# Optimization experiments

Hardware: AMD Instinct MI355X
Metric: run time of the kernel (lower is better)

Reference implementation:

```python
import jax, jax.numpy as jnp
import numpy as np

NF, NH, NC, B = 8, 200, 8, 131072  # nFeatures, nHidden, nCls, batch
NEQ = 2

def _lin_init(k, fan_in, fan_out):
    k1, k2 = jax.random.split(k)
    s = 1.0 / np.sqrt(fan_in)
    W = jax.random.uniform(k1, (fan_out, fan_in), minval=-s, maxval=s, dtype=jnp.float32)
    b = jax.random.uniform(k2, (fan_out,), minval=-s, maxval=s, dtype=jnp.float32)
    return W, b

def setup_inputs() -> dict:
    key = jax.random.key(0)
    ks = jax.random.split(key, 6)
    W0, b0 = _lin_init(ks[0], NF, NF)
    W1, b1 = _lin_init(ks[1], NF, NH)
    W2, b2 = _lin_init(ks[2], NH, NH)
    W3, b3 = _lin_init(ks[3], NH, NH)
    W4, b4 = _lin_init(ks[4], NH, NC)
    Q = jnp.eye(NF, dtype=jnp.float32)  # Parameter initialized to identity
    x = jax.random.normal(ks[5], (B, NF), dtype=jnp.float32)
    return dict(x=x, Q=Q, W0=W0, b0=b0, W1=W1, b1=b1, W2=W2, b2=b2, W3=W3, b3=b3, W4=W4, b4=b4)

def _qp_equality(Q, p, A, bvec):
    # min 1/2 z'Qz + p'z  s.t.  A z = b.  (G=0, h=0 => inequality constraints vacuous.)
    # KKT: [Q A'; A 0] [z; nu] = [-p; b], solved batched (tiny 10x10 systems).
    Bn, m, n = A.shape
    Qb = jnp.broadcast_to(Q, (Bn, n, n))
    K = jnp.concatenate([
        jnp.concatenate([Qb, jnp.swapaxes(A, 1, 2)], axis=2),        # [B, n, n+m]
        jnp.concatenate([A, jnp.zeros((Bn, m, m), Q.dtype)], axis=2) # [B, m, n+m]
    ], axis=1)                                                        # [B, n+m, n+m]
    rhs = jnp.concatenate([-p, bvec], axis=1)                         # [B, n+m]
    sol = jnp.linalg.solve(K, rhs[..., None])[..., 0]
    return sol[:, :n]

def reference(x, Q, W0, b0, W1, b1, W2, b2, W3, b3, W4, b4):
    h = x @ W0.T + b0                      # fc0, [B, 8]
    p = -h
    z_ = jnp.zeros_like(h[:, 3])
    o_ = jnp.ones_like(h[:, 3])
    # A[i] = [[0,0,0,0,h[i,3],1,0,0], [0,0,0,0,0,0,h[i,3],1]]  (detached in original)
    A = jnp.stack([
        jnp.stack([z_, z_, z_, z_, h[:, 3], o_, z_, z_], axis=1),
        jnp.stack([z_, z_, z_, z_, z_, z_, h[:, 3], o_], axis=1)], axis=1)  # [B, 2, 8]
    A = jax.lax.stop_gradient(A)  # torch.tensor(...) breaks the graph for A
    bvec = jnp.stack([h[:, 3] * h[:, 4] + h[:, 5],
                      h[:, 3] * h[:, 6] + h[:, 7]], axis=1)  # [B, 2]
    z = _qp_equality(Q, p, A, bvec)        # QPFunction solution, [B, 8]
    y = jax.nn.relu(z @ W1.T + b1)
    y = jax.nn.relu(y @ W2.T + b2)
    y = jax.nn.relu(y @ W3.T + b3)
    return y @ W4.T + b4                   # [B, 8]
```

## Files before the change

kernel.cpp:

```cpp
#include <hip/hip_runtime.h>
#include <math.h>

typedef _Float16 f16;
typedef f16 half8 __attribute__((ext_vector_type(8)));
typedef float floatx4 __attribute__((ext_vector_type(4)));

#define NF 8
#define NH 200
#define NC 8
#define ACT_W 232
#define ROWS 64
#define CHUNK 4
#define OUTP_W 9
#define FRAG 512

#define WS_QI   0
#define WS_B1P  256
#define WS_B2P  1152
#define WS_B3P  2048
#define WS_WP1  3008
#define WS_WP2  16320
#define WS_WP3  109504
#define WS_WP4  202688
#define WS_NEED 212000

__device__ __forceinline__ void pack_frag(const float* __restrict__ W, int Nv, int Kv,
                                          int nkt, int nks, f16* __restrict__ dst, int gid)
{
    if (gid < nks * nkt * 64) {
        const int ks    = gid / (nkt * 64);
        const int rem   = gid - ks * nkt * 64;
        const int nt    = rem >> 6;
        const int lane  = rem & 63;
        const int n     = nt * 16 + (lane & 15);
        const int kbase = ks * 32 + ((lane >> 4) * 8);
        f16 tmp[8];
#pragma unroll
        for (int j = 0; j < 8; ++j) {
            const int k = kbase + j;
            tmp[j] = (n < Nv && k < Kv) ? (f16)W[n * Kv + k] : (f16)0.0f;
        }
        *(half8*)&dst[(size_t)gid * 8] = *(const half8*)tmp;
    }
}

__global__ void prep_kernel(const float* __restrict__ Q,
                            const float* __restrict__ W1, const float* __restrict__ b1,
                            const float* __restrict__ W2, const float* __restrict__ b2,
                            const float* __restrict__ W3, const float* __restrict__ b3,
                            const float* __restrict__ W4,
                            char* __restrict__ ws)
{
    const int gid = blockIdx.x * 256 + threadIdx.x;
    pack_frag(W1, NH, NF, 13, 1, (f16*)(ws + WS_WP1), gid);
    pack_frag(W2, NH, NH, 13, 7, (f16*)(ws + WS_WP2), gid);
    pack_frag(W3, NH, NH, 13, 7, (f16*)(ws + WS_WP3), gid);
    pack_frag(W4, NC, NH, 1,  7, (f16*)(ws + WS_WP4), gid);
    if (gid < 224) {
        ((float*)(ws + WS_B1P))[gid] = (gid < NH) ? b1[gid] : 0.0f;
        ((float*)(ws + WS_B2P))[gid] = (gid < NH) ? b2[gid] : 0.0f;
        ((float*)(ws + WS_B3P))[gid] = (gid < NH) ? b3[gid] : 0.0f;
    }

    if (blockIdx.x == 0) {
        __shared__ float aug[8][16];
        __shared__ int piv;
        float* Qi = (float*)(ws + WS_QI);
        const int t  = threadIdx.x;
        const bool a = t < 128;
        const int r  = (t >> 4) & 7;
        const int c2 = t & 15;
        if (a) aug[r][c2] = (c2 < 8) ? Q[r * 8 + c2] : ((c2 - 8 == r) ? 1.0f : 0.0f);
        __syncthreads();
        for (int c = 0; c < 8; ++c) {
            if (t == 0) {
                int p = c; float best = fabsf(aug[c][c]);
                for (int rr = c + 1; rr < 8; ++rr) {
                    float v = fabsf(aug[rr][c]);
                    if (v > best) { best = v; p = rr; }
                }
                piv = p;
            }
            __syncthreads();
            const int p = piv;
            float myv = a ? aug[r][c2] : 0.0f;
            __syncthreads();
            if (a) {
                if (r == c)      aug[p][c2] = myv;
                else if (r == p) aug[c][c2] = myv;
            }
            __syncthreads();
            const float pv = aug[c][c];
            __syncthreads();
            if (a && r == c) aug[r][c2] = aug[r][c2] / pv;
            __syncthreads();
            const float fac  = (a && r != c) ? aug[r][c] : 0.0f;
            const float prow = aug[c][c2];
            __syncthreads();
            if (a) aug[r][c2] -= fac * prow;
            __syncthreads();
        }
        if (a && c2 >= 8) Qi[r * 8 + (c2 - 8)] = aug[r][c2];
    }
}

__device__ __forceinline__ half8 ldf(const f16* __restrict__ p, int lane)
{
    return *(const half8*)&p[lane * 8];
}

template<int TC>
__device__ __forceinline__ void run_path(
    const float* __restrict__ x,
    const float* __restrict__ W0, const float* __restrict__ b0,
    const float* __restrict__ b4,
    const char* __restrict__ ws,
    float* __restrict__ out, int B,
    f16* __restrict__ actA, f16* __restrict__ actB,
    f16* __restrict__ zbuf, float* __restrict__ outP,
    const int wid, const int lane, const int c, const int g, const int t0)
{
    const float* Qi  = (const float*)(ws + WS_QI);
    const float* b1p = (const float*)(ws + WS_B1P);
    const float* b2p = (const float*)(ws + WS_B2P);
    const float* b3p = (const float*)(ws + WS_B3P);
    const f16*  Wp1  = (const f16*)(ws + WS_WP1);
    const f16*  Wp2  = (const f16*)(ws + WS_WP2);
    const f16*  Wp3  = (const f16*)(ws + WS_WP3);
    const f16*  Wp4  = (const f16*)(ws + WS_WP4);

    half8 wf1[TC], wf2[TC][7], wf3[TC][7];
    float bv1[TC], bv2[TC], bv3[TC];
#pragma unroll
    for (int t = 0; t < TC; ++t) {
        wf1[t] = ldf(Wp1 + (size_t)(t0 + t) * FRAG, lane);
#pragma unroll
        for (int ks = 0; ks < 7; ++ks) {
            wf2[t][ks] = ldf(Wp2 + (size_t)(ks * 13 + t0 + t) * FRAG, lane);
            wf3[t][ks] = ldf(Wp3 + (size_t)(ks * 13 + t0 + t) * FRAG, lane);
        }
        bv1[t] = b1p[(t0 + t) * 16 + c];
        bv2[t] = b2p[(t0 + t) * 16 + c];
        bv3[t] = b3p[(t0 + t) * 16 + c];
    }
    const bool doL4 = (wid < 7);
    half8 w4f = {};
    if (doL4) w4f = ldf(Wp4 + (size_t)wid * FRAG, lane);

    const long blockbase = (long)blockIdx.x * (ROWS * CHUNK);
    const int  tid = wid * 64 + lane;

    if (tid < 256) {
        f16* buf = (tid & 128) ? actB : actA;
        const int row  = (tid >> 1) & 63;
        const int part = tid & 1;
        half8 zz = {};
        *(half8*)&buf[row * ACT_W + 208 + part * 8] = zz;
    }

    float xr[NF];
#pragma unroll
    for (int i = 0; i < NF; ++i) xr[i] = 0.0f;
    if (wid == 0) {
        const long gr = blockbase + lane;
        if (gr < B) {
            const float4* xp = (const float4*)(x + gr * NF);
            const float4 A = xp[0], Bv = xp[1];
            xr[0] = A.x; xr[1] = A.y; xr[2] = A.z; xr[3] = A.w;
            xr[4] = Bv.x; xr[5] = Bv.y; xr[6] = Bv.z; xr[7] = Bv.w;
        }
    }

#pragma unroll 1
    for (int ck = 0; ck < CHUNK; ++ck) {
        const long base = blockbase + (long)ck * ROWS;

        if (wid == 0) {
            float xn[NF];
#pragma unroll
            for (int i = 0; i < NF; ++i) xn[i] = 0.0f;
            if (ck + 1 < CHUNK) {
                const long gn = base + ROWS + lane;
                if (gn < B) {
                    const float4* xp = (const float4*)(x + gn * NF);
                    const float4 A = xp[0], Bv = xp[1];
                    xn[0] = A.x; xn[1] = A.y; xn[2] = A.z; xn[3] = A.w;
                    xn[4] = Bv.x; xn[5] = Bv.y; xn[6] = Bv.z; xn[7] = Bv.w;
                }
            }
            float h[NF];
#pragma unroll
            for (int j = 0; j < NF; ++j) {
                float acc = b0[j];
#pragma unroll
                for (int k = 0; k < NF; ++k) acc = fmaf(W0[j * NF + k], xr[k], acc);
                h[j] = acc;
            }
            float tq[NF], u0[NF], u1[NF];
            const float h3 = h[3];
#pragma unroll
            for (int i = 0; i < NF; ++i) {
                float s = 0.0f;
#pragma unroll
                for (int k = 0; k < NF; ++k) s = fmaf(Qi[i * NF + k], h[k], s);
                tq[i] = s;
                u0[i] = fmaf(Qi[i * NF + 4], h3, Qi[i * NF + 5]);
                u1[i] = fmaf(Qi[i * NF + 6], h3, Qi[i * NF + 7]);
            }
            const float m00 = fmaf(h3, u0[4], u0[5]);
            const float m01 = fmaf(h3, u1[4], u1[5]);
            const float m10 = fmaf(h3, u0[6], u0[7]);
            const float m11 = fmaf(h3, u1[6], u1[7]);
            const float r0  = fmaf(h3, tq[4], tq[5]) - fmaf(h3, h[4], h[5]);
            const float r1  = fmaf(h3, tq[6], tq[7]) - fmaf(h3, h[6], h[7]);
            const float idet = 1.0f / (m00 * m11 - m01 * m10);
            const float nu0 = (m11 * r0 - m01 * r1) * idet;
            const float nu1 = (m00 * r1 - m10 * r0) * idet;
            half8 zh, zz = {};
#pragma unroll
            for (int k = 0; k < 8; ++k) zh[k] = (f16)(tq[k] - u0[k] * nu0 - u1[k] * nu1);
            *(half8*)&zbuf[lane * 32 + 0]  = zh;
            *(half8*)&zbuf[lane * 32 + 8]  = zz;
            *(half8*)&zbuf[lane * 32 + 16] = zz;
            *(half8*)&zbuf[lane * 32 + 24] = zz;
#pragma unroll
            for (int i = 0; i < NF; ++i) xr[i] = xn[i];
        }
        __syncthreads();

#pragma unroll
        for (int m = 0; m < 4; ++m) {
            const half8 az = *(const half8*)&zbuf[(m * 16 + c) * 32 + g * 8];
#pragma unroll
            for (int t = 0; t < TC; ++t) {
                floatx4 acc;
                acc[0] = bv1[t]; acc[1] = bv1[t]; acc[2] = bv1[t]; acc[3] = bv1[t];
                acc = __builtin_amdgcn_mfma_f32_16x16x32_f16(az, wf1[t], acc, 0, 0, 0);
#pragma unroll
                for (int r = 0; r < 4; ++r)
                    actA[(m * 16 + g * 4 + r) * ACT_W + (t0 + t) * 16 + c] =
                        (f16)fmaxf(acc[r], 0.0f);
            }
        }
        __syncthreads();

#pragma unroll
        for (int m = 0; m < 4; ++m) {
            half8 af[7];
#pragma unroll
            for (int ks = 0; ks < 7; ++ks)
                af[ks] = *(const half8*)&actA[(m * 16 + c) * ACT_W + ks * 32 + g * 8];
#pragma unroll
            for (int t = 0; t < TC; ++t) {
                floatx4 acc;
                acc[0] = bv2[t]; acc[1] = bv2[t]; acc[2] = bv2[t]; acc[3] = bv2[t];
#pragma unroll
                for (int ks = 0; ks < 7; ++ks)
                    acc = __builtin_amdgcn_mfma_f32_16x16x32_f16(af[ks], wf2[t][ks], acc, 0, 0, 0);
#pragma unroll
                for (int r = 0; r < 4; ++r)
                    actB[(m * 16 + g * 4 + r) * ACT_W + (t0 + t) * 16 + c] =
                        (f16)fmaxf(acc[r], 0.0f);
            }
        }
        __syncthreads();

#pragma unroll
        for (int m = 0; m < 4; ++m) {
            half8 af[7];
#pragma unroll
            for (int ks = 0; ks < 7; ++ks)
                af[ks] = *(const half8*)&actB[(m * 16 + c) * ACT_W + ks * 32 + g * 8];
#pragma unroll
            for (int t = 0; t < TC; ++t) {
                floatx4 acc;
                acc[0] = bv3[t]; acc[1] = bv3[t]; acc[2] = bv3[t]; acc[3] = bv3[t];
#pragma unroll
                for (int ks = 0; ks < 7; ++ks)
                    acc = __builtin_amdgcn_mfma_f32_16x16x32_f16(af[ks], wf3[t][ks], acc, 0, 0, 0);
#pragma unroll
                for (int r = 0; r < 4; ++r)
                    actA[(m * 16 + g * 4 + r) * ACT_W + (t0 + t) * 16 + c] =
                        (f16)fmaxf(acc[r], 0.0f);
            }
        }
        __syncthreads();

        if (doL4) {
#pragma unroll
            for (int m = 0; m < 4; ++m) {
                const half8 af = *(const half8*)&actA[(m * 16 + c) * ACT_W + wid * 32 + g * 8];
                floatx4 a4 = {};
                a4 = __builtin_amdgcn_mfma_f32_16x16x32_f16(af, w4f, a4, 0, 0, 0);
                if (c < NC) {
#pragma unroll
                    for (int r = 0; r < 4; ++r)
                        outP[(wid * ROWS + m * 16 + g * 4 + r) * OUTP_W + c] = a4[r];
                }
            }
        }
        __syncthreads();

        if (tid < 256) {
            const int e   = tid * 2;
            const int row = e >> 3;
            const int col = e & 7;
            float s0 = b4[col], s1 = b4[col + 1];
#pragma unroll
            for (int w = 0; w < 7; ++w) {
                s0 += outP[(w * ROWS + row) * OUTP_W + col];
                s1 += outP[(w * ROWS + row) * OUTP_W + col + 1];
            }
            const long gr = base + row;
            if (gr < B) {
                float2 v; v.x = s0; v.y = s1;
                *(float2*)&out[gr * NC + col] = v;
            }
        }
    }
}

__global__ __launch_bounds__(512, 2)
void mlp_pers(const float* __restrict__ x,
              const float* __restrict__ W0, const float* __restrict__ b0,
              const float* __restrict__ b4,
              const char* __restrict__ ws,
              float* __restrict__ out, int B)
{
    __shared__ f16   actA[ROWS * ACT_W];
    __shared__ f16   actB[ROWS * ACT_W];
    __shared__ f16   zbuf[ROWS * 32];
    __shared__ float outP[7 * ROWS * OUTP_W];

    const int tid  = threadIdx.x;
    const int lane = tid & 63;
    const int wid  = __builtin_amdgcn_readfirstlane(tid >> 6);
    const int c    = lane & 15;
    const int g    = lane >> 4;

    if (wid < 5)
        run_path<2>(x, W0, b0, b4, ws, out, B, actA, actB, zbuf, outP,
                    wid, lane, c, g, 2 * wid);
    else
        run_path<1>(x, W0, b0, b4, ws, out, B, actA, actB, zbuf, outP,
                    wid, lane, c, g, wid + 5);
}

#define BT 64
#define NWAVE 8
#define JB 25
#define CH 8

__device__ __forceinline__ void layer200(const float* __restrict__ in_,
                                         float* __restrict__ out_,
                                         const float* __restrict__ W,
                                         const float* __restrict__ bias,
                                         int j0, int lane)
{
    float acc[JB];
#pragma unroll
    for (int jj = 0; jj < JB; ++jj) acc[jj] = bias[j0 + jj];
#pragma unroll 1
    for (int k0 = 0; k0 < NH; k0 += CH) {
        float a[CH];
#pragma unroll
        for (int u = 0; u < CH; ++u) a[u] = in_[(k0 + u) * BT + lane];
#pragma unroll
        for (int jj = 0; jj < JB; ++jj) {
            const float* wr = W + (j0 + jj) * NH + k0;
#pragma unroll
            for (int u = 0; u < CH; ++u) acc[jj] = fmaf(wr[u], a[u], acc[jj]);
        }
    }
#pragma unroll
    for (int jj = 0; jj < JB; ++jj)
        out_[(j0 + jj) * BT + lane] = fmaxf(acc[jj], 0.0f);
}

__global__ void qinv_kernel(const float* __restrict__ Q, float* __restrict__ Qi)
{
    __shared__ float aug[8][16];
    __shared__ int piv;
    const int t  = threadIdx.x;
    const int r  = t >> 4;
    const int c2 = t & 15;
    aug[r][c2] = (c2 < 8) ? Q[r * 8 + c2] : ((c2 - 8 == r) ? 1.0f : 0.0f);
    __syncthreads();
    for (int c = 0; c < 8; ++c) {
        if (t == 0) {
            int p = c; float best = fabsf(aug[c][c]);
            for (int rr = c + 1; rr < 8; ++rr) {
                float v = fabsf(aug[rr][c]);
                if (v > best) { best = v; p = rr; }
            }
            piv = p;
        }
        __syncthreads();
        const int p = piv;
        float myv = aug[r][c2];
        __syncthreads();
        if (r == c)      aug[p][c2] = myv;
        else if (r == p) aug[c][c2] = myv;
        __syncthreads();
        const float pv = aug[c][c];
        __syncthreads();
        if (r == c) aug[r][c2] = aug[r][c2] / pv;
        __syncthreads();
        const float fac  = (r == c) ? 0.0f : aug[r][c];
        const float prow = aug[c][c2];
        __syncthreads();
        aug[r][c2] -= fac * prow;
        __syncthreads();
    }
    if (c2 >= 8) Qi[r * 8 + (c2 - 8)] = aug[r][c2];
}

__global__ __launch_bounds__(BT * NWAVE, 2)
void mlp_fused(const float* __restrict__ x, const float* __restrict__ Qi,
               const float* __restrict__ W0, const float* __restrict__ b0,
               const float* __restrict__ W1, const float* __restrict__ b1,
               const float* __restrict__ W2, const float* __restrict__ b2,
               const float* __restrict__ W3, const float* __restrict__ b3,
               const float* __restrict__ W4, const float* __restrict__ b4,
               float* __restrict__ out, int B)
{
    __shared__ float actA[NH * BT];
    __shared__ float actB[NH * BT];
    __shared__ float outP[NWAVE * NC * BT];

    const int lane = threadIdx.x & 63;
    const int wid  = __builtin_amdgcn_readfirstlane((int)(threadIdx.x >> 6));
    const int g    = blockIdx.x * BT + lane;
    const int j0   = wid * JB;

    float xr[NF];
    if (g < B) {
        const float4* xp = reinterpret_cast<const float4*>(x + (size_t)g * NF);
        float4 x0 = xp[0], x1 = xp[1];
        xr[0] = x0.x; xr[1] = x0.y; xr[2] = x0.z; xr[3] = x0.w;
        xr[4] = x1.x; xr[5] = x1.y; xr[6] = x1.z; xr[7] = x1.w;
    } else {
#pragma unroll
        for (int i = 0; i < NF; ++i) xr[i] = 0.0f;
    }
    float h[NF];
#pragma unroll
    for (int j = 0; j < NF; ++j) {
        float acc = b0[j];
#pragma unroll
        for (int k = 0; k < NF; ++k) acc = fmaf(W0[j * NF + k], xr[k], acc);
        h[j] = acc;
    }
    float tq[NF], u0[NF], u1[NF];
    const float h3 = h[3];
#pragma unroll
    for (int i = 0; i < NF; ++i) {
        float s = 0.0f;
#pragma unroll
        for (int k = 0; k < NF; ++k) s = fmaf(Qi[i * NF + k], h[k], s);
        tq[i] = s;
        u0[i] = fmaf(Qi[i * NF + 4], h3, Qi[i * NF + 5]);
        u1[i] = fmaf(Qi[i * NF + 6], h3, Qi[i * NF + 7]);
    }
    const float m00 = fmaf(h3, u0[4], u0[5]);
    const float m01 = fmaf(h3, u1[4], u1[5]);
    const float m10 = fmaf(h3, u0[6], u0[7]);
    const float m11 = fmaf(h3, u1[6], u1[7]);
    const float r0  = fmaf(h3, tq[4], tq[5]) - fmaf(h3, h[4], h[5]);
    const float r1  = fmaf(h3, tq[6], tq[7]) - fmaf(h3, h[6], h[7]);
    const float idet = 1.0f / (m00 * m11 - m01 * m10);
    const float nu0 = (m11 * r0 - m01 * r1) * idet;
    const float nu1 = (m00 * r1 - m10 * r0) * idet;
    float z[NF];
#pragma unroll
    for (int i = 0; i < NF; ++i) z[i] = tq[i] - u0[i] * nu0 - u1[i] * nu1;

#pragma unroll
    for (int jj = 0; jj < JB; ++jj) {
        const int j = j0 + jj;
        float acc = b1[j];
#pragma unroll
        for (int k = 0; k < NF; ++k) acc = fmaf(W1[j * NF + k], z[k], acc);
        actA[j * BT + lane] = fmaxf(acc, 0.0f);
    }
    __syncthreads();
    layer200(actA, actB, W2, b2, j0, lane);
    __syncthreads();
    layer200(actB, actA, W3, b3, j0, lane);
    __syncthreads();
    {
        float a[JB];
#pragma unroll
        for (int kk = 0; kk < JB; ++kk) a[kk] = actA[(j0 + kk) * BT + lane];
        float acc[NC];
#pragma unroll
        for (int o = 0; o < NC; ++o) acc[o] = 0.0f;
#pragma unroll
        for (int o = 0; o < NC; ++o) {
            const float* wr = W4 + o * NH + j0;
#pragma unroll
            for (int kk = 0; kk < JB; ++kk) acc[o] = fmaf(wr[kk], a[kk], acc[o]);
        }
#pragma unroll
        for (int o = 0; o < NC; ++o) outP[(wid * NC + o) * BT + lane] = acc[o];
    }
    __syncthreads();
    {
        float s = b4[wid];
#pragma unroll
        for (int w = 0; w < NWAVE; ++w) s += outP[(w * NC + wid) * BT + lane];
        if (g < B) out[(size_t)g * NC + wid] = s;
    }
}

extern "C" void kernel_launch(void* const* d_in, const int* in_sizes, int n_in,
                              void* d_out, int out_size, void* d_ws, size_t ws_size,
                              hipStream_t stream)
{
    const float* x  = (const float*)d_in[0];
    const float* Q  = (const float*)d_in[1];
    const float* W0 = (const float*)d_in[2];
    const float* b0 = (const float*)d_in[3];
    const float* W1 = (const float*)d_in[4];
    const float* b1 = (const float*)d_in[5];
    const float* W2 = (const float*)d_in[6];
    const float* b2 = (const float*)d_in[7];
    const float* W3 = (const float*)d_in[8];
    const float* b3 = (const float*)d_in[9];
    const float* W4 = (const float*)d_in[10];
    const float* b4 = (const float*)d_in[11];
    float* out = (float*)d_out;

    const int B = in_sizes[0] / NF;

    if (ws_size >= WS_NEED) {
        hipLaunchKernelGGL(prep_kernel, dim3(23), dim3(256), 0, stream,
                           Q, W1, b1, W2, b2, W3, b3, W4, (char*)d_ws);
        const int nblk = (B + ROWS * CHUNK - 1) / (ROWS * CHUNK);
        hipLaunchKernelGGL(mlp_pers, dim3(nblk), dim3(512), 0, stream,
                           x, W0, b0, b4, (const char*)d_ws, out, B);
    } else {
        float* Qi = (float*)d_ws;
        hipLaunchKernelGGL(qinv_kernel, dim3(1), dim3(128), 0, stream, Q, Qi);
        hipLaunchKernelGGL(mlp_fused, dim3((B + BT - 1) / BT), dim3(BT * NWAVE), 0, stream,
                           x, Qi, W0, b0, W1, b1, W2, b2, W3, b3, W4, b4, out, B);
    }
}
```

Baseline: 57.71 us.

## Switch MLP layers to 32x32x16 MFMA with 128-row tiles and swizzled LDS

Replaces the 16x16x32 MFMA path with 32x32x16 MFMA tiles, where each of 7 waves owns a 32-column slice of the hidden layer. Weights are repacked in the prep kernel to match. Rows per chunk double to 128, and activation stores and loads use an XOR swizzle to avoid LDS bank conflicts. The goal is better MFMA efficiency, with register-resident weights reused over more rows and two accumulators interleaved to hide MFMA latency. The cost is higher register and LDS pressure: LDS nearly doubles, which may cap occupancy at 2 blocks per CU.

```diff
diff --git a/kernel.cpp b/kernel.cpp
--- a/kernel.cpp
+++ b/kernel.cpp
@@ -4,12 +4,14 @@
 typedef _Float16 f16;
 typedef f16 half8 __attribute__((ext_vector_type(8)));
 typedef float floatx4 __attribute__((ext_vector_type(4)));
+typedef float floatx16 __attribute__((ext_vector_type(16)));
 
 #define NF 8
 #define NH 200
 #define NC 8
 #define ACT_W 232
-#define ROWS 64
+#define ZB_W 40
+#define ROWS 128
 #define CHUNK 4
 #define OUTP_W 9
 #define FRAG 512
@@ -18,11 +20,11 @@
 #define WS_B1P  256
 #define WS_B2P  1152
 #define WS_B3P  2048
-#define WS_WP1  3008
-#define WS_WP2  16320
-#define WS_WP3  109504
-#define WS_WP4  202688
-#define WS_NEED 212000
+#define WS_W1P  2944
+#define WS_W2P  10112
+#define WS_W3P  110464
+#define WS_W4P  210816
+#define WS_NEED 217984
 
 __device__ __forceinline__ void pack_frag(const float* __restrict__ W, int Nv, int Kv,
                                           int nkt, int nks, f16* __restrict__ dst, int gid)
@@ -44,6 +46,26 @@
     }
 }
 
+__device__ __forceinline__ void pack32(const float* __restrict__ W, int Nv, int Kv,
+                                       int nks, f16* __restrict__ dst, int gid)
+{
+    if (gid < nks * 7 * 64) {
+        const int ks    = gid / 448;
+        const int rem   = gid - ks * 448;
+        const int nt    = rem >> 6;
+        const int lane  = rem & 63;
+        const int n     = nt * 32 + (lane & 31);
+        const int kbase = ks * 16 + ((lane >> 5) * 8);
+        f16 tmp[8];
+#pragma unroll
+        for (int j = 0; j < 8; ++j) {
+            const int k = kbase + j;
+            tmp[j] = (n < Nv && k < Kv) ? (f16)W[n * Kv + k] : (f16)0.0f;
+        }
+        *(half8*)&dst[(size_t)gid * 8] = *(const half8*)tmp;
+    }
+}
+
 __global__ void prep_kernel(const float* __restrict__ Q,
                             const float* __restrict__ W1, const float* __restrict__ b1,
                             const float* __restrict__ W2, const float* __restrict__ b2,
@@ -52,10 +74,10 @@
                             char* __restrict__ ws)
 {
     const int gid = blockIdx.x * 256 + threadIdx.x;
-    pack_frag(W1, NH, NF, 13, 1, (f16*)(ws + WS_WP1), gid);
-    pack_frag(W2, NH, NH, 13, 7, (f16*)(ws + WS_WP2), gid);
-    pack_frag(W3, NH, NH, 13, 7, (f16*)(ws + WS_WP3), gid);
-    pack_frag(W4, NC, NH, 1,  7, (f16*)(ws + WS_WP4), gid);
+    pack32(W1, NH, NF, 1,  (f16*)(ws + WS_W1P), gid);
+    pack32(W2, NH, NH, 14, (f16*)(ws + WS_W2P), gid);
+    pack32(W3, NH, NH, 14, (f16*)(ws + WS_W3P), gid);
+    pack_frag(W4, NC, NH, 1, 7, (f16*)(ws + WS_W4P), gid);
     if (gid < 224) {
         ((float*)(ws + WS_B1P))[gid] = (gid < NH) ? b1[gid] : 0.0f;
         ((float*)(ws + WS_B2P))[gid] = (gid < NH) ? b2[gid] : 0.0f;
@@ -109,60 +131,65 @@
     return *(const half8*)&p[lane * 8];
 }
 
-template<int TC>
-__device__ __forceinline__ void run_path(
-    const float* __restrict__ x,
-    const float* __restrict__ W0, const float* __restrict__ b0,
-    const float* __restrict__ b4,
-    const char* __restrict__ ws,
-    float* __restrict__ out, int B,
-    f16* __restrict__ actA, f16* __restrict__ actB,
-    f16* __restrict__ zbuf, float* __restrict__ outP,
-    const int wid, const int lane, const int c, const int g, const int t0)
-{
+__global__ __launch_bounds__(448, 2)
+void mlp32(const float* __restrict__ x,
+           const float* __restrict__ W0, const float* __restrict__ b0,
+           const float* __restrict__ b4,
+           const char* __restrict__ ws,
+           float* __restrict__ out, int B)
+{
+    __shared__ f16   actA[ROWS * ACT_W];
+    __shared__ f16   actB[ROWS * ACT_W];
+    __shared__ f16   zbuf[ROWS * ZB_W];
+    __shared__ float outP[7 * ROWS * OUTP_W];
+
+    const int tid  = threadIdx.x;
+    const int lane = tid & 63;
+    const int wid  = __builtin_amdgcn_readfirstlane(tid >> 6);
+    const int l31  = lane & 31;
+    const int h    = lane >> 5;
+    const int c    = lane & 15;
+    const int g    = lane >> 4;
+    const int s    = (l31 >> 3) & 3;
+
     const float* Qi  = (const float*)(ws + WS_QI);
     const float* b1p = (const float*)(ws + WS_B1P);
     const float* b2p = (const float*)(ws + WS_B2P);
     const float* b3p = (const float*)(ws + WS_B3P);
-    const f16*  Wp1  = (const f16*)(ws + WS_WP1);
-    const f16*  Wp2  = (const f16*)(ws + WS_WP2);
-    const f16*  Wp3  = (const f16*)(ws + WS_WP3);
-    const f16*  Wp4  = (const f16*)(ws + WS_WP4);
-
-    half8 wf1[TC], wf2[TC][7], wf3[TC][7];
-    float bv1[TC], bv2[TC], bv3[TC];
-#pragma unroll
-    for (int t = 0; t < TC; ++t) {
-        wf1[t] = ldf(Wp1 + (size_t)(t0 + t) * FRAG, lane);
-#pragma unroll
-        for (int ks = 0; ks < 7; ++ks) {
-            wf2[t][ks] = ldf(Wp2 + (size_t)(ks * 13 + t0 + t) * FRAG, lane);
-            wf3[t][ks] = ldf(Wp3 + (size_t)(ks * 13 + t0 + t) * FRAG, lane);
-        }
-        bv1[t] = b1p[(t0 + t) * 16 + c];
-        bv2[t] = b2p[(t0 + t) * 16 + c];
-        bv3[t] = b3p[(t0 + t) * 16 + c];
-    }
-    const bool doL4 = (wid < 7);
-    half8 w4f = {};
-    if (doL4) w4f = ldf(Wp4 + (size_t)wid * FRAG, lane);
+    const f16*  W1p  = (const f16*)(ws + WS_W1P);
+    const f16*  W2p  = (const f16*)(ws + WS_W2P);
+    const f16*  W3p  = (const f16*)(ws + WS_W3P);
+    const f16*  W4p  = (const f16*)(ws + WS_W4P);
+
+    half8 wf2[14], wf3[14];
+#pragma unroll
+    for (int ks = 0; ks < 14; ++ks) {
+        wf2[ks] = ldf(W2p + (size_t)(ks * 7 + wid) * FRAG, lane);
+        wf3[ks] = ldf(W3p + (size_t)(ks * 7 + wid) * FRAG, lane);
+    }
+    const half8 wf1 = ldf(W1p + (size_t)wid * FRAG, lane);
+    const half8 w4f = ldf(W4p + (size_t)wid * FRAG, lane);
+    const float bv1 = b1p[wid * 32 + l31];
+    const float bv2 = b2p[wid * 32 + l31];
+    const float bv3 = b3p[wid * 32 + l31];
+
+    if (tid < 256) {
+        const int row = tid & 127;
+        f16* buf = (tid & 128) ? actB : actA;
+        const int sw = (row >> 3) & 3;
+        half8 zz = {};
+        *(half8*)&buf[row * ACT_W + ((26 ^ sw) << 3)] = zz;
+        *(half8*)&buf[row * ACT_W + ((27 ^ sw) << 3)] = zz;
+    }
 
     const long blockbase = (long)blockIdx.x * (ROWS * CHUNK);
-    const int  tid = wid * 64 + lane;
-
-    if (tid < 256) {
-        f16* buf = (tid & 128) ? actB : actA;
-        const int row  = (tid >> 1) & 63;
-        const int part = tid & 1;
-        half8 zz = {};
-        *(half8*)&buf[row * ACT_W + 208 + part * 8] = zz;
-    }
+    const int  hrow = wid * 64 + lane;
 
     float xr[NF];
 #pragma unroll
     for (int i = 0; i < NF; ++i) xr[i] = 0.0f;
-    if (wid == 0) {
-        const long gr = blockbase + lane;
+    if (wid < 2) {
+        const long gr = blockbase + hrow;
         if (gr < B) {
             const float4* xp = (const float4*)(x + gr * NF);
             const float4 A = xp[0], Bv = xp[1];
@@ -175,12 +202,12 @@
     for (int ck = 0; ck < CHUNK; ++ck) {
         const long base = blockbase + (long)ck * ROWS;
 
-        if (wid == 0) {
+        if (wid < 2) {
             float xn[NF];
 #pragma unroll
             for (int i = 0; i < NF; ++i) xn[i] = 0.0f;
             if (ck + 1 < CHUNK) {
-                const long gn = base + ROWS + lane;
+                const long gn = base + ROWS + hrow;
                 if (gn < B) {
                     const float4* xp = (const float4*)(x + gn * NF);
                     const float4 A = xp[0], Bv = xp[1];
@@ -188,22 +215,22 @@
                     xn[4] = Bv.x; xn[5] = Bv.y; xn[6] = Bv.z; xn[7] = Bv.w;
                 }
             }
-            float h[NF];
+            float hh[NF];
 #pragma unroll
             for (int j = 0; j < NF; ++j) {
                 float acc = b0[j];
 #pragma unroll
                 for (int k = 0; k < NF; ++k) acc = fmaf(W0[j * NF + k], xr[k], acc);
-                h[j] = acc;
+                hh[j] = acc;
             }
             float tq[NF], u0[NF], u1[NF];
-            const float h3 = h[3];
+            const float h3 = hh[3];
 #pragma unroll
             for (int i = 0; i < NF; ++i) {
-                float s = 0.0f;
-#pragma unroll
-                for (int k = 0; k < NF; ++k) s = fmaf(Qi[i * NF + k], h[k], s);
-                tq[i] = s;
+                float ss = 0.0f;
+#pragma unroll
+                for (int k = 0; k < NF; ++k) ss = fmaf(Qi[i * NF + k], hh[k], ss);
+                tq[i] = ss;
                 u0[i] = fmaf(Qi[i * NF + 4], h3, Qi[i * NF + 5]);
                 u1[i] = fmaf(Qi[i * NF + 6], h3, Qi[i * NF + 7]);
             }
@@ -211,18 +238,16 @@
             const float m01 = fmaf(h3, u1[4], u1[5]);
             const float m10 = fmaf(h3, u0[6], u0[7]);
             const float m11 = fmaf(h3, u1[6], u1[7]);
-            const float r0  = fmaf(h3, tq[4], tq[5]) - fmaf(h3, h[4], h[5]);
-            const float r1  = fmaf(h3, tq[6], tq[7]) - fmaf(h3, h[6], h[7]);
+            const float r0  = fmaf(h3, tq[4], tq[5]) - fmaf(h3, hh[4], hh[5]);
+            const float r1  = fmaf(h3, tq[6], tq[7]) - fmaf(h3, hh[6], hh[7]);
             const float idet = 1.0f / (m00 * m11 - m01 * m10);
             const float nu0 = (m11 * r0 - m01 * r1) * idet;
             const float nu1 = (m00 * r1 - m10 * r0) * idet;
             half8 zh, zz = {};
 #pragma unroll
             for (int k = 0; k < 8; ++k) zh[k] = (f16)(tq[k] - u0[k] * nu0 - u1[k] * nu1);
-            *(half8*)&zbuf[lane * 32 + 0]  = zh;
-            *(half8*)&zbuf[lane * 32 + 8]  = zz;
-            *(half8*)&zbuf[lane * 32 + 16] = zz;
-            *(half8*)&zbuf[lane * 32 + 24] = zz;
+            *(half8*)&zbuf[hrow * ZB_W + 0] = zh;
+            *(half8*)&zbuf[hrow * ZB_W + 8] = zz;
 #pragma unroll
             for (int i = 0; i < NF; ++i) xr[i] = xn[i];
         }
@@ -230,120 +255,109 @@
 
 #pragma unroll
         for (int m = 0; m < 4; ++m) {
-            const half8 az = *(const half8*)&zbuf[(m * 16 + c) * 32 + g * 8];
-#pragma unroll
-            for (int t = 0; t < TC; ++t) {
-                floatx4 acc;
-                acc[0] = bv1[t]; acc[1] = bv1[t]; acc[2] = bv1[t]; acc[3] = bv1[t];
-                acc = __builtin_amdgcn_mfma_f32_16x16x32_f16(az, wf1[t], acc, 0, 0, 0);
-#pragma unroll
-                for (int r = 0; r < 4; ++r)
-                    actA[(m * 16 + g * 4 + r) * ACT_W + (t0 + t) * 16 + c] =
-                        (f16)fmaxf(acc[r], 0.0f);
+            const half8 az = *(const half8*)&zbuf[(m * 32 + l31) * ZB_W + h * 8];
+            floatx16 a0;
+#pragma unroll
+            for (int i = 0; i < 16; ++i) a0[i] = bv1;
+            a0 = __builtin_amdgcn_mfma_f32_32x32x16_f16(az, wf1, a0, 0, 0, 0);
+            const int chunkw = wid * 4 + (l31 >> 3);
+#pragma unroll
+            for (int rr = 0; rr < 16; ++rr) {
+                const int row = m * 32 + (rr & 3) + 8 * (rr >> 2) + 4 * h;
+                actA[row * ACT_W + (((chunkw ^ (rr >> 2)) << 3) | (l31 & 7))] =
+                    (f16)fmaxf(a0[rr], 0.0f);
             }
         }
         __syncthreads();
 
 #pragma unroll
         for (int m = 0; m < 4; ++m) {
-            half8 af[7];
-#pragma unroll
-            for (int ks = 0; ks < 7; ++ks)
-                af[ks] = *(const half8*)&actA[(m * 16 + c) * ACT_W + ks * 32 + g * 8];
-#pragma unroll
-            for (int t = 0; t < TC; ++t) {
-                floatx4 acc;
-                acc[0] = bv2[t]; acc[1] = bv2[t]; acc[2] = bv2[t]; acc[3] = bv2[t];
-#pragma unroll
-                for (int ks = 0; ks < 7; ++ks)
-                    acc = __builtin_amdgcn_mfma_f32_16x16x32_f16(af[ks], wf2[t][ks], acc, 0, 0, 0);
-#pragma unroll
-                for (int r = 0; r < 4; ++r)
-                    actB[(m * 16 + g * 4 + r) * ACT_W + (t0 + t) * 16 + c] =
-                        (f16)fmaxf(acc[r], 0.0f);
+            const int rowa = (m * 32 + l31) * ACT_W;
+            half8 af[14];
+#pragma unroll
+            for (int ks = 0; ks < 14; ++ks)
+                af[ks] = *(const half8*)&actA[rowa + (((ks * 2 + h) ^ s) << 3)];
+            floatx16 e0, e1;
+#pragma unroll
+            for (int i = 0; i < 16; ++i) { e0[i] = bv2; e1[i] = 0.0f; }
+#pragma unroll
+            for (int ks = 0; ks < 14; ks += 2) {
+                e0 = __builtin_amdgcn_mfma_f32_32x32x16_f16(af[ks],     wf2[ks],     e0, 0, 0, 0);
+                e1 = __builtin_amdgcn_mfma_f32_32x32x16_f16(af[ks + 1], wf2[ks + 1], e1, 0, 0, 0);
+            }
+            const int chunkw = wid * 4 + (l31 >> 3);
+#pragma unroll
+            for (int rr = 0; rr < 16; ++rr) {
+                const int row = m * 32 + (rr & 3) + 8 * (rr >> 2) + 4 * h;
+                actB[row * ACT_W + (((chunkw ^ (rr >> 2)) << 3) | (l31 & 7))] =
+                    (f16)fmaxf(e0[rr] + e1[rr], 0.0f);
             }
         }
         __syncthreads();
 
 #pragma unroll
         for (int m = 0; m < 4; ++m) {
-            half8 af[7];
-#pragma unroll
-            for (int ks = 0; ks < 7; ++ks)
-                af[ks] = *(const half8*)&actB[(m * 16 + c) * ACT_W + ks * 32 + g * 8];
-#pragma unroll
-            for (int t = 0; t < TC; ++t) {
-                floatx4 acc;
-                acc[0] = bv3[t]; acc[1] = bv3[t]; acc[2] = bv3[t]; acc[3] = bv3[t];
-#pragma unroll
-                for (int ks = 0; ks < 7; ++ks)
-                    acc = __builtin_amdgcn_mfma_f32_16x16x32_f16(af[ks], wf3[t][ks], acc, 0, 0, 0);
-#pragma unroll
-                for (int r = 0; r < 4; ++r)
-                    actA[(m * 16 + g * 4 + r) * ACT_W + (t0 + t) * 16 + c] =
-                        (f16)fmaxf(acc[r], 0.0f);
-            }
-        }
-        __syncthreads();
-
-        if (doL4) {
-#pragma unroll
-            for (int m = 0; m < 4; ++m) {
-                const half8 af = *(const half8*)&actA[(m * 16 + c) * ACT_W + wid * 32 + g * 8];
+            const int rowa = (m * 32 + l31) * ACT_W;
+            half8 af[14];
+#pragma unroll
+            for (int ks = 0; ks < 14; ++ks)
+                af[ks] = *(const half8*)&actB[rowa + (((ks * 2 + h) ^ s) << 3)];
+            floatx16 e0, e1;
+#pragma unroll
+            for (int i = 0; i < 16; ++i) { e0[i] = bv3; e1[i] = 0.0f; }
+#pragma unroll
+            for (int ks = 0; ks < 14; ks += 2) {
+                e0 = __builtin_amdgcn_mfma_f32_32x32x16_f16(af[ks],     wf3[ks],     e0, 0, 0, 0);
+                e1 = __builtin_amdgcn_mfma_f32_32x32x16_f16(af[ks + 1], wf3[ks + 1], e1, 0, 0, 0);
+            }
+            const int chunkw = wid * 4 + (l31 >> 3);
+#pragma unroll
+            for (int rr = 0; rr < 16; ++rr) {
+                const int row = m * 32 + (rr & 3) + 8 * (rr >> 2) + 4 * h;
+                actA[row * ACT_W + (((chunkw ^ (rr >> 2)) << 3) | (l31 & 7))] =
+                    (f16)fmaxf(e0[rr] + e1[rr], 0.0f);
+            }
+        }
+        __syncthreads();
+
+        {
+#pragma unroll
+            for (int m16 = 0; m16 < 8; ++m16) {
+                const int row = m16 * 16 + c;
+                const int sw  = (row >> 3) & 3;
+                const int chunk = wid * 4 + g;
+                const half8 af = *(const half8*)&actA[row * ACT_W + (((chunk ^ sw) << 3))];
                 floatx4 a4 = {};
                 a4 = __builtin_amdgcn_mfma_f32_16x16x32_f16(af, w4f, a4, 0, 0, 0);
                 if (c < NC) {
 #pragma unroll
                     for (int r = 0; r < 4; ++r)
-                        outP[(wid * ROWS + m * 16 + g * 4 + r) * OUTP_W + c] = a4[r];
+                        outP[(wid * ROWS + m16 * 16 + g * 4 + r) * OUTP_W + c] = a4[r];
                 }
             }
         }
         __syncthreads();
 
         if (tid < 256) {
-            const int e   = tid * 2;
-            const int row = e >> 3;
-            const int col = e & 7;
-            float s0 = b4[col], s1 = b4[col + 1];
-#pragma unroll
-            for (int w = 0; w < 7; ++w) {
-                s0 += outP[(w * ROWS + row) * OUTP_W + col];
-                s1 += outP[(w * ROWS + row) * OUTP_W + col + 1];
-            }
-            const long gr = base + row;
-            if (gr < B) {
-                float2 v; v.x = s0; v.y = s1;
-                *(float2*)&out[gr * NC + col] = v;
-            }
-        }
-    }
-}
-
-__global__ __launch_bounds__(512, 2)
-void mlp_pers(const float* __restrict__ x,
-              const float* __restrict__ W0, const float* __restrict__ b0,
-              const float* __restrict__ b4,
-              const char* __restrict__ ws,
-              float* __restrict__ out, int B)
-{
-    __shared__ f16   actA[ROWS * ACT_W];
-    __shared__ f16   actB[ROWS * ACT_W];
-    __shared__ f16   zbuf[ROWS * 32];
-    __shared__ float outP[7 * ROWS * OUTP_W];
-
-    const int tid  = threadIdx.x;
-    const int lane = tid & 63;
-    const int wid  = __builtin_amdgcn_readfirstlane(tid >> 6);
-    const int c    = lane & 15;
-    const int g    = lane >> 4;
-
-    if (wid < 5)
-        run_path<2>(x, W0, b0, b4, ws, out, B, actA, actB, zbuf, outP,
-                    wid, lane, c, g, 2 * wid);
-    else
-        run_path<1>(x, W0, b0, b4, ws, out, B, actA, actB, zbuf, outP,
-                    wid, lane, c, g, wid + 5);
+#pragma unroll
+            for (int half = 0; half < 2; ++half) {
+                const int e   = (tid + half * 256) * 2;
+                const int row = e >> 3;
+                const int col = e & 7;
+                float s0 = b4[col], s1 = b4[col + 1];
+#pragma unroll
+                for (int w = 0; w < 7; ++w) {
+                    s0 += outP[(w * ROWS + row) * OUTP_W + col];
+                    s1 += outP[(w * ROWS + row) * OUTP_W + col + 1];
+                }
+                const long gr = base + row;
+                if (gr < B) {
+                    float2 v; v.x = s0; v.y = s1;
+                    *(float2*)&out[gr * NC + col] = v;
+                }
+            }
+        }
+    }
 }
 
 #define BT 64
@@ -534,10 +548,10 @@
     const int B = in_sizes[0] / NF;
 
     if (ws_size >= WS_NEED) {
-        hipLaunchKernelGGL(prep_kernel, dim3(23), dim3(256), 0, stream,
+        hipLaunchKernelGGL(prep_kernel, dim3(25), dim3(256), 0, stream,
                            Q, W1, b1, W2, b2, W3, b3, W4, (char*)d_ws);
         const int nblk = (B + ROWS * CHUNK - 1) / (ROWS * CHUNK);
-        hipLaunchKernelGGL(mlp_pers, dim3(nblk), dim3(512), 0, stream,
+        hipLaunchKernelGGL(mlp32, dim3(nblk), dim3(448), 0, stream,
                            x, W0, b0, b4, (const char*)d_ws, out, B);
     } else {
         float* Qi = (float*)d_ws;
```

Result: slower. 81.94 us (+42.0%).

## Stream weight fragments per chunk instead of register-resident, raise occupancy target

Applied to the files above, without the earlier changes.

Weight fragments for layers 1-4 are no longer preloaded into registers once per block. They are reloaded from global/L2 inside each chunk iteration. Layers 2 and 3 are restructured to loop over k-steps with four row-tile accumulators that share one weight fragment. The launch bounds go from 2 to 4 blocks per CU, trading register pressure for repeated weight loads. LDS usage is about 76KB per block, so four blocks may not fit and the real occupancy gain may be limited.

```diff
diff --git a/kernel.cpp b/kernel.cpp
--- a/kernel.cpp
+++ b/kernel.cpp
@@ -9,6 +9,7 @@
 #define NH 200
 #define NC 8
 #define ACT_W 232
+#define ZB_W 32
 #define ROWS 64
 #define CHUNK 4
 #define OUTP_W 9
@@ -107,6 +108,37 @@
 __device__ __forceinline__ half8 ldf(const f16* __restrict__ p, int lane)
 {
     return *(const half8*)&p[lane * 8];
+}
+
+__device__ __forceinline__ void tile_col(const f16* __restrict__ Wp, int tile,
+                                         const float bias,
+                                         const f16* __restrict__ src,
+                                         f16* __restrict__ dst,
+                                         const int lane, const int c, const int g)
+{
+    floatx4 acc[4];
+#pragma unroll
+    for (int m = 0; m < 4; ++m) {
+        floatx4 v; v[0] = bias; v[1] = bias; v[2] = bias; v[3] = bias;
+        acc[m] = v;
+    }
+#pragma unroll
+    for (int ks = 0; ks < 7; ++ks) {
+        const half8 fb = ldf(Wp + (size_t)(ks * 13 + tile) * FRAG, lane);
+        half8 af[4];
+#pragma unroll
+        for (int m = 0; m < 4; ++m)
+            af[m] = *(const half8*)&src[(m * 16 + c) * ACT_W + ks * 32 + g * 8];
+#pragma unroll
+        for (int m = 0; m < 4; ++m)
+            acc[m] = __builtin_amdgcn_mfma_f32_16x16x32_f16(af[m], fb, acc[m], 0, 0, 0);
+    }
+#pragma unroll
+    for (int m = 0; m < 4; ++m)
+#pragma unroll
+        for (int r = 0; r < 4; ++r)
+            dst[(m * 16 + g * 4 + r) * ACT_W + tile * 16 + c] =
+                (f16)fmaxf(acc[m][r], 0.0f);
 }
 
 template<int TC>
@@ -129,24 +161,7 @@
     const f16*  Wp3  = (const f16*)(ws + WS_WP3);
     const f16*  Wp4  = (const f16*)(ws + WS_WP4);
 
-    half8 wf1[TC], wf2[TC][7], wf3[TC][7];
-    float bv1[TC], bv2[TC], bv3[TC];
-#pragma unroll
-    for (int t = 0; t < TC; ++t) {
-        wf1[t] = ldf(Wp1 + (size_t)(t0 + t) * FRAG, lane);
-#pragma unroll
-        for (int ks = 0; ks < 7; ++ks) {
-            wf2[t][ks] = ldf(Wp2 + (size_t)(ks * 13 + t0 + t) * FRAG, lane);
-            wf3[t][ks] = ldf(Wp3 + (size_t)(ks * 13 + t0 + t) * FRAG, lane);
-        }
-        bv1[t] = b1p[(t0 + t) * 16 + c];
-        bv2[t] = b2p[(t0 + t) * 16 + c];
-        bv3[t] = b3p[(t0 + t) * 16 + c];
-    }
     const bool doL4 = (wid < 7);
-    half8 w4f = {};
-    if (doL4) w4f = ldf(Wp4 + (size_t)wid * FRAG, lane);
-
     const long blockbase = (long)blockIdx.x * (ROWS * CHUNK);
     const int  tid = wid * 64 + lane;
 
@@ -219,23 +234,25 @@
             half8 zh, zz = {};
 #pragma unroll
             for (int k = 0; k < 8; ++k) zh[k] = (f16)(tq[k] - u0[k] * nu0 - u1[k] * nu1);
-            *(half8*)&zbuf[lane * 32 + 0]  = zh;
-            *(half8*)&zbuf[lane * 32 + 8]  = zz;
-            *(half8*)&zbuf[lane * 32 + 16] = zz;
-            *(half8*)&zbuf[lane * 32 + 24] = zz;
+            *(half8*)&zbuf[lane * ZB_W + 0]  = zh;
+            *(half8*)&zbuf[lane * ZB_W + 8]  = zz;
+            *(half8*)&zbuf[lane * ZB_W + 16] = zz;
+            *(half8*)&zbuf[lane * ZB_W + 24] = zz;
 #pragma unroll
             for (int i = 0; i < NF; ++i) xr[i] = xn[i];
         }
         __syncthreads();
 
 #pragma unroll
-        for (int m = 0; m < 4; ++m) {
-            const half8 az = *(const half8*)&zbuf[(m * 16 + c) * 32 + g * 8];
-#pragma unroll
-            for (int t = 0; t < TC; ++t) {
+        for (int t = 0; t < TC; ++t) {
+            const half8 fb = ldf(Wp1 + (size_t)(t0 + t) * FRAG, lane);
+            const float bias = b1p[(t0 + t) * 16 + c];
+#pragma unroll
+            for (int m = 0; m < 4; ++m) {
+                const half8 az = *(const half8*)&zbuf[(m * 16 + c) * ZB_W + g * 8];
                 floatx4 acc;
-                acc[0] = bv1[t]; acc[1] = bv1[t]; acc[2] = bv1[t]; acc[3] = bv1[t];
-                acc = __builtin_amdgcn_mfma_f32_16x16x32_f16(az, wf1[t], acc, 0, 0, 0);
+                acc[0] = bias; acc[1] = bias; acc[2] = bias; acc[3] = bias;
+                acc = __builtin_amdgcn_mfma_f32_16x16x32_f16(az, fb, acc, 0, 0, 0);
 #pragma unroll
                 for (int r = 0; r < 4; ++r)
                     actA[(m * 16 + g * 4 + r) * ACT_W + (t0 + t) * 16 + c] =
@@ -245,48 +262,17 @@
         __syncthreads();
 
 #pragma unroll
-        for (int m = 0; m < 4; ++m) {
-            half8 af[7];
-#pragma unroll
-            for (int ks = 0; ks < 7; ++ks)
-                af[ks] = *(const half8*)&actA[(m * 16 + c) * ACT_W + ks * 32 + g * 8];
-#pragma unroll
-            for (int t = 0; t < TC; ++t) {
-                floatx4 acc;
-                acc[0] = bv2[t]; acc[1] = bv2[t]; acc[2] = bv2[t]; acc[3] = bv2[t];
-#pragma unroll
-                for (int ks = 0; ks < 7; ++ks)
-                    acc = __builtin_amdgcn_mfma_f32_16x16x32_f16(af[ks], wf2[t][ks], acc, 0, 0, 0);
-#pragma unroll
-                for (int r = 0; r < 4; ++r)
-                    actB[(m * 16 + g * 4 + r) * ACT_W + (t0 + t) * 16 + c] =
-                        (f16)fmaxf(acc[r], 0.0f);
-            }
-        }
-        __syncthreads();
-
-#pragma unroll
-        for (int m = 0; m < 4; ++m) {
-            half8 af[7];
-#pragma unroll
-            for (int ks = 0; ks < 7; ++ks)
-                af[ks] = *(const half8*)&actB[(m * 16 + c) * ACT_W + ks * 32 + g * 8];
-#pragma unroll
-            for (int t = 0; t < TC; ++t) {
-                floatx4 acc;
-                acc[0] = bv3[t]; acc[1] = bv3[t]; acc[2] = bv3[t]; acc[3] = bv3[t];
-#pragma unroll
-                for (int ks = 0; ks < 7; ++ks)
-                    acc = __builtin_amdgcn_mfma_f32_16x16x32_f16(af[ks], wf3[t][ks], acc, 0, 0, 0);
-#pragma unroll
-                for (int r = 0; r < 4; ++r)
-                    actA[(m * 16 + g * 4 + r) * ACT_W + (t0 + t) * 16 + c] =
-                        (f16)fmaxf(acc[r], 0.0f);
-            }
-        }
+        for (int t = 0; t < TC; ++t)
+            tile_col(Wp2, t0 + t, b2p[(t0 + t) * 16 + c], actA, actB, lane, c, g);
+        __syncthreads();
+
+#pragma unroll
+        for (int t = 0; t < TC; ++t)
+            tile_col(Wp3, t0 + t, b3p[(t0 + t) * 16 + c], actB, actA, lane, c, g);
         __syncthreads();
 
         if (doL4) {
+            const half8 w4f = ldf(Wp4 + (size_t)wid * FRAG, lane);
 #pragma unroll
             for (int m = 0; m < 4; ++m) {
                 const half8 af = *(const half8*)&actA[(m * 16 + c) * ACT_W + wid * 32 + g * 8];
@@ -320,8 +306,8 @@
     }
 }
 
-__global__ __launch_bounds__(512, 2)
-void mlp_pers(const float* __restrict__ x,
+__global__ __launch_bounds__(512, 4)
+void mlp_lean(const float* __restrict__ x,
               const float* __restrict__ W0, const float* __restrict__ b0,
               const float* __restrict__ b4,
               const char* __restrict__ ws,
@@ -329,7 +315,7 @@
 {
     __shared__ f16   actA[ROWS * ACT_W];
     __shared__ f16   actB[ROWS * ACT_W];
-    __shared__ f16   zbuf[ROWS * 32];
+    __shared__ f16   zbuf[ROWS * ZB_W];
     __shared__ float outP[7 * ROWS * OUTP_W];
 
     const int tid  = threadIdx.x;
@@ -537,7 +523,7 @@
         hipLaunchKernelGGL(prep_kernel, dim3(23), dim3(256), 0, stream,
                            Q, W1, b1, W2, b2, W3, b3, W4, (char*)d_ws);
         const int nblk = (B + ROWS * CHUNK - 1) / (ROWS * CHUNK);
-        hipLaunchKernelGGL(mlp_pers, dim3(nblk), dim3(512), 0, stream,
+        hipLaunchKernelGGL(mlp_lean, dim3(nblk), dim3(512), 0, stream,
                            x, W0, b0, b4, (const char*)d_ws, out, B);
     } else {
         float* Qi = (float*)d_ws;
```

Measured after the change: 86.65 us. +50.1%, slower.
